# Performance work log

Measured on AMD Instinct MI355X. Metric: run time of the kernel, lower is better.

The kernel has to match this reference:

```python
import jax, jax.numpy as jnp
import numpy as np

N_NODES = 50000
N_EDGES = 800000
N_GRAPHS = 256
F_IN = 32
HEADS = 8
NEG_SLOPE = 0.2


def gat_conv(x, W, a_src, a_dst, bias, src, dst, n_nodes, heads, ch):
    # x: [N, Fin], W: [Fin, heads*ch], a_src/a_dst: [heads, ch], bias: [heads*ch]
    h = (x @ W).reshape(n_nodes, heads, ch)              # [N,H,C]
    alpha_src = jnp.sum(h * a_src, axis=-1)              # [N,H]
    alpha_dst = jnp.sum(h * a_dst, axis=-1)              # [N,H]
    logit = alpha_src[src] + alpha_dst[dst]              # [E,H]
    logit = jax.nn.leaky_relu(logit, NEG_SLOPE)
    # segment softmax over edges grouped by destination node
    m = jax.ops.segment_max(logit, dst, num_segments=n_nodes)   # [N,H]
    m = jnp.where(jnp.isfinite(m), m, 0.0)
    e = jnp.exp(logit - m[dst])                          # [E,H]
    denom = jax.ops.segment_sum(e, dst, num_segments=n_nodes)   # [N,H]
    alpha = e / (denom[dst] + 1e-16)                     # [E,H]
    msg = h[src] * alpha[:, :, None]                     # [E,H,C]
    out = jax.ops.segment_sum(msg, dst, num_segments=n_nodes)   # [N,H,C]
    return out.reshape(n_nodes, heads * ch) + bias


def setup_inputs() -> dict:
    key = jax.random.key(0)
    ks = jax.random.split(key, 20)
    H = HEADS
    glorot = lambda k, shape: jax.random.normal(k, shape, jnp.float32) * (2.0 / (shape[0] + shape[-1])) ** 0.5
    inp = {
        "x": jax.random.normal(ks[0], (N_NODES, F_IN), jnp.float32),
        "W1": glorot(ks[1], (F_IN, H * 8)),
        "a_src1": glorot(ks[2], (H, 8)),
        "a_dst1": glorot(ks[3], (H, 8)),
        "b1": jnp.zeros((H * 8,), jnp.float32),
        "W2": glorot(ks[4], (64, H * 16)),
        "a_src2": glorot(ks[5], (H, 16)),
        "a_dst2": glorot(ks[6], (H, 16)),
        "b2": jnp.zeros((H * 16,), jnp.float32),
        "W3": glorot(ks[7], (128, H * 16)),
        "a_src3": glorot(ks[8], (H, 16)),
        "a_dst3": glorot(ks[9], (H, 16)),
        "b3": jnp.zeros((H * 16,), jnp.float32),
        "fc1_w": glorot(ks[10], (128, 10)),
        "fc1_b": jnp.zeros((10,), jnp.float32),
        "fc2_w": glorot(ks[11], (10, 1)),
        "fc2_b": jnp.zeros((1,), jnp.float32),
        "edge_index": jax.random.randint(ks[12], (2, N_EDGES), 0, N_NODES, jnp.int64 if jax.config.jax_enable_x64 else jnp.int32),
        "batch_vec": jnp.sort(jax.random.randint(ks[13], (N_NODES,), 0, N_GRAPHS, jnp.int32)),
        "num_graphs": N_GRAPHS,
    }
    return inp


def reference(x, W1, a_src1, a_dst1, b1, W2, a_src2, a_dst2, b2,
              W3, a_src3, a_dst3, b3, fc1_w, fc1_b, fc2_w, fc2_b,
              edge_index, batch_vec, num_graphs):
    n = x.shape[0]
    loops = jnp.arange(n, dtype=edge_index.dtype)
    src = jnp.concatenate([edge_index[0], loops])  # PyG GATConv add_self_loops=True
    dst = jnp.concatenate([edge_index[1], loops])

    h = jax.nn.elu(gat_conv(x, W1, a_src1, a_dst1, b1, src, dst, n, HEADS, 8))
    h = jax.nn.elu(gat_conv(h, W2, a_src2, a_dst2, b2, src, dst, n, HEADS, 16))
    h = jax.nn.elu(gat_conv(h, W3, a_src3, a_dst3, b3, src, dst, n, HEADS, 16))

    # global mean pool over graphs
    sums = jax.ops.segment_sum(h, batch_vec, num_segments=num_graphs)
    counts = jax.ops.segment_sum(jnp.ones((n,), h.dtype), batch_vec, num_segments=num_graphs)
    pooled = sums / jnp.maximum(counts, 1.0)[:, None]   # [G,128]

    z = jax.nn.relu(pooled @ fc1_w + fc1_b)
    return z @ fc2_w + fc2_b                             # [G,1]
```

## Files before the change

kernel.cpp:

```cpp
#include <hip/hip_runtime.h>
#include <hip/hip_bf16.h>

#define N_NODES   50000
#define N_EDGES   800000
#define N_TOT     850000
#define N_GRAPHS  256
#define HEADS     8
#define NEG_SLOPE 0.2f

template<int FIN, int FOUT>
__global__ __launch_bounds__(256) void gemm_kernel(const float* __restrict__ X,
                                                   const float* __restrict__ W,
                                                   float* __restrict__ H) {
    constexpr int KC    = 32;
    constexpr int THR_F = FOUT / 4;
    constexpr int NPT   = 64 / (256 / THR_F);
    constexpr int XS_S  = 68;
    __shared__ float xs[KC * XS_S];
    __shared__ float ws[KC * FOUT];
    const int t = threadIdx.x;
    const int node0 = blockIdx.x * 64;
    const int fo  = (t % THR_F) * 4;
    const int ndb = (t / THR_F) * NPT;
    float4 acc[NPT];
#pragma unroll
    for (int i = 0; i < NPT; ++i) acc[i] = make_float4(0.f, 0.f, 0.f, 0.f);

    const int xn = t >> 2, ks = (t & 3) * 8;
    for (int kc = 0; kc < FIN; kc += KC) {
        __syncthreads();
        float4 a0 = make_float4(0.f,0.f,0.f,0.f), a1 = a0;
        if (node0 + xn < N_NODES) {
            const float* xp = X + (size_t)(node0 + xn) * FIN + kc + ks;
            a0 = *(const float4*)xp;
            a1 = *(const float4*)(xp + 4);
        }
        xs[(ks + 0) * XS_S + xn] = a0.x;
        xs[(ks + 1) * XS_S + xn] = a0.y;
        xs[(ks + 2) * XS_S + xn] = a0.z;
        xs[(ks + 3) * XS_S + xn] = a0.w;
        xs[(ks + 4) * XS_S + xn] = a1.x;
        xs[(ks + 5) * XS_S + xn] = a1.y;
        xs[(ks + 6) * XS_S + xn] = a1.z;
        xs[(ks + 7) * XS_S + xn] = a1.w;
        constexpr int WF4 = KC * FOUT / 4 / 256;
        const float4* wsrc = (const float4*)(W + (size_t)kc * FOUT);
        float4* wdst = (float4*)ws;
#pragma unroll
        for (int i = 0; i < WF4; ++i) wdst[t * WF4 + i] = wsrc[t * WF4 + i];
        __syncthreads();
#pragma unroll 4
        for (int k = 0; k < KC; ++k) {
            float4 wv = *(const float4*)(ws + k * FOUT + fo);
#pragma unroll
            for (int q = 0; q < NPT / 4; ++q) {
                float4 xv = *(const float4*)(xs + k * XS_S + ndb + q * 4);
                acc[q*4+0].x += xv.x * wv.x; acc[q*4+0].y += xv.x * wv.y;
                acc[q*4+0].z += xv.x * wv.z; acc[q*4+0].w += xv.x * wv.w;
                acc[q*4+1].x += xv.y * wv.x; acc[q*4+1].y += xv.y * wv.y;
                acc[q*4+1].z += xv.y * wv.z; acc[q*4+1].w += xv.y * wv.w;
                acc[q*4+2].x += xv.z * wv.x; acc[q*4+2].y += xv.z * wv.y;
                acc[q*4+2].z += xv.z * wv.z; acc[q*4+2].w += xv.z * wv.w;
                acc[q*4+3].x += xv.w * wv.x; acc[q*4+3].y += xv.w * wv.y;
                acc[q*4+3].z += xv.w * wv.z; acc[q*4+3].w += xv.w * wv.w;
            }
        }
    }
#pragma unroll
    for (int i = 0; i < NPT; ++i) {
        int row = node0 + ndb + i;
        if (row < N_NODES) *(float4*)(H + (size_t)row * FOUT + fo) = acc[i];
    }
}

template<int CH>
__global__ void alpha_kernel(const float* __restrict__ H,
                             const float* __restrict__ a_src,
                             const float* __restrict__ a_dst,
                             float* __restrict__ asrc, float* __restrict__ adst) {
    int tid = blockIdx.x * blockDim.x + threadIdx.x;
    if (tid >= N_NODES * HEADS) return;
    int n = tid / HEADS, h = tid % HEADS;
    const float4* hp = (const float4*)(H + (size_t)n * (HEADS * CH) + h * CH);
    const float4* as = (const float4*)(a_src + h * CH);
    const float4* ad = (const float4*)(a_dst + h * CH);
    float s = 0.f, d = 0.f;
#pragma unroll
    for (int c = 0; c < CH / 4; ++c) {
        float4 v = hp[c], a = as[c], b = ad[c];
        s += v.x * a.x + v.y * a.y + v.z * a.z + v.w * a.w;
        d += v.x * b.x + v.y * b.y + v.z * b.z + v.w * b.w;
    }
    asrc[tid] = s;
    adst[tid] = d;
}

__global__ void hist_kernel(const int* __restrict__ edst, int* __restrict__ cnt) {
    int e = blockIdx.x * blockDim.x + threadIdx.x;
    if (e >= N_TOT) return;
    int d = (e < N_EDGES) ? edst[e] : e - N_EDGES;
    atomicAdd(&cnt[d], 1);
}

__global__ void scan1_kernel(const int* __restrict__ cnt, int* __restrict__ excl,
                             int* __restrict__ bsum) {
    __shared__ int sm[256];
    int t = threadIdx.x;
    int i = blockIdx.x * 256 + t;
    int v = (i < N_NODES) ? cnt[i] : 0;
    sm[t] = v;
    __syncthreads();
    for (int off = 1; off < 256; off <<= 1) {
        int x = (t >= off) ? sm[t - off] : 0;
        __syncthreads();
        sm[t] += x;
        __syncthreads();
    }
    if (i < N_NODES) excl[i] = sm[t] - v;
    if (t == 255) bsum[blockIdx.x] = sm[255];
}

__global__ void scan2_kernel(int* __restrict__ bsum, int nblk) {
    __shared__ int sm[256];
    int t = threadIdx.x;
    int v = (t < nblk) ? bsum[t] : 0;
    sm[t] = v;
    __syncthreads();
    for (int off = 1; off < 256; off <<= 1) {
        int x = (t >= off) ? sm[t - off] : 0;
        __syncthreads();
        sm[t] += x;
        __syncthreads();
    }
    if (t < nblk) bsum[t] = sm[t] - v;
}

__global__ void scan3_kernel(const int* __restrict__ excl, const int* __restrict__ bsum,
                             int* __restrict__ row_ptr) {
    int i = blockIdx.x * blockDim.x + threadIdx.x;
    if (i < N_NODES) row_ptr[i] = excl[i] + bsum[i >> 8];
    if (i == N_NODES) row_ptr[N_NODES] = N_TOT;
}

__global__ void scatter_kernel(const int* __restrict__ esrc, const int* __restrict__ edst,
                               const int* __restrict__ row_ptr, int* __restrict__ cursor,
                               int* __restrict__ edge_src) {
    int e = blockIdx.x * blockDim.x + threadIdx.x;
    if (e >= N_TOT) return;
    int s, d;
    if (e < N_EDGES) { s = esrc[e]; d = edst[e]; } else { s = d = e - N_EDGES; }
    int pos = row_ptr[d] + atomicAdd(&cursor[d], 1);
    edge_src[pos] = s;
}

template<int CH>
__global__ __launch_bounds__(256) void gat_gather_kernel(
        const int* __restrict__ row_ptr, const int* __restrict__ edge_src,
        const float* __restrict__ asrc, const float* __restrict__ adst,
        const float* __restrict__ H, const float* __restrict__ bias,
        float* __restrict__ out) {
    constexpr int LPE   = 2 * CH;
    constexpr int SPLIT = 64 / LPE;
    constexpr int LPH   = CH / 4;
    constexpr int HS    = 8 * CH;
    const int n = (blockIdx.x * blockDim.x + threadIdx.x) >> 6;
    if (n >= N_NODES) return;
    const int lane = threadIdx.x & 63;
    const int sub = lane / LPE;
    const int li  = lane & (LPE - 1);
    const int h   = li / LPH;
    const int off = h * CH + (li & (LPH - 1)) * 4;
    const float adst_h = adst[n * 8 + h];
    const int e0 = row_ptr[n], e1 = row_ptr[n + 1];
    float sum = 0.f;
    float4 acc = make_float4(0.f, 0.f, 0.f, 0.f);
    int e = e0 + sub;
    for (; e + SPLIT < e1; e += 2 * SPLIT) {
        int s0 = edge_src[e];
        int s1 = edge_src[e + SPLIT];
        float l0 = asrc[s0 * 8 + h] + adst_h;
        float l1 = asrc[s1 * 8 + h] + adst_h;
        float4 h0 = *(const float4*)(H + (size_t)s0 * HS + off);
        float4 h1 = *(const float4*)(H + (size_t)s1 * HS + off);
        l0 = l0 > 0.f ? l0 : NEG_SLOPE * l0;
        l1 = l1 > 0.f ? l1 : NEG_SLOPE * l1;
        float w0 = __expf(l0), w1 = __expf(l1);
        sum += w0 + w1;
        acc.x += w0 * h0.x + w1 * h1.x;
        acc.y += w0 * h0.y + w1 * h1.y;
        acc.z += w0 * h0.z + w1 * h1.z;
        acc.w += w0 * h0.w + w1 * h1.w;
    }
    if (e < e1) {
        int s = edge_src[e];
        float l = asrc[s * 8 + h] + adst_h;
        float4 hv = *(const float4*)(H + (size_t)s * HS + off);
        l = l > 0.f ? l : NEG_SLOPE * l;
        float w = __expf(l);
        sum += w;
        acc.x += w * hv.x;
        acc.y += w * hv.y;
        acc.z += w * hv.z;
        acc.w += w * hv.w;
    }
#pragma unroll
    for (int mask = LPE; mask < 64; mask <<= 1) {
        sum   += __shfl_xor(sum, mask, 64);
        acc.x += __shfl_xor(acc.x, mask, 64);
        acc.y += __shfl_xor(acc.y, mask, 64);
        acc.z += __shfl_xor(acc.z, mask, 64);
        acc.w += __shfl_xor(acc.w, mask, 64);
    }
    float inv = 1.0f / (sum + 1e-16f);
    float4 bv = *(const float4*)(bias + off);
    float4 v;
    v.x = acc.x * inv + bv.x;  v.x = v.x > 0.f ? v.x : expm1f(v.x);
    v.y = acc.y * inv + bv.y;  v.y = v.y > 0.f ? v.y : expm1f(v.y);
    v.z = acc.z * inv + bv.z;  v.z = v.z > 0.f ? v.z : expm1f(v.z);
    v.w = acc.w * inv + bv.w;  v.w = v.w > 0.f ? v.w : expm1f(v.w);
    *(float4*)(out + (size_t)n * HS + off) = v;
}

__global__ void gstart_kernel(const int* __restrict__ batch, int* __restrict__ gstart) {
    int g = threadIdx.x;
    int lo = 0, hi = N_NODES;
    while (lo < hi) {
        int mid = (lo + hi) >> 1;
        if (batch[mid] < g) lo = mid + 1; else hi = mid;
    }
    gstart[g] = lo;
    if (g == 0) gstart[N_GRAPHS] = N_NODES;
}

__global__ __launch_bounds__(512) void pool_head_kernel(
        const float* __restrict__ act, const int* __restrict__ gstart,
        const float* __restrict__ fc1_w, const float* __restrict__ fc1_b,
        const float* __restrict__ fc2_w, const float* __restrict__ fc2_b,
        float* __restrict__ out) {
    int g = blockIdx.x;
    int t = threadIdx.x;
    int f = t & 127, strip = t >> 7;
    int n0 = gstart[g], n1 = gstart[g + 1];
    float s = 0.f;
    for (int n = n0 + strip; n < n1; n += 4) s += act[(size_t)n * 128 + f];
    __shared__ float sm[4][128];
    __shared__ float zz[10];
    sm[strip][f] = s;
    __syncthreads();
    if (strip == 0) {
        float cnt = (float)(n1 - n0);
        cnt = cnt > 1.f ? cnt : 1.f;
        sm[0][f] = (sm[0][f] + sm[1][f] + sm[2][f] + sm[3][f]) / cnt;
    }
    __syncthreads();
    if (t < 10) {
        float z = fc1_b[t];
        for (int q = 0; q < 128; ++q) z += sm[0][q] * fc1_w[q * 10 + t];
        zz[t] = z > 0.f ? z : 0.f;
    }
    __syncthreads();
    if (t == 0) {
        float o = fc2_b[0];
#pragma unroll
        for (int j = 0; j < 10; ++j) o += zz[j] * fc2_w[j];
        out[g] = o;
    }
}

extern "C" void kernel_launch(void* const* d_in, const int* in_sizes, int n_in,
                              void* d_out, int out_size, void* d_ws, size_t ws_size,
                              hipStream_t stream) {
    const float* x      = (const float*)d_in[0];
    const float* W1     = (const float*)d_in[1];
    const float* a_src1 = (const float*)d_in[2];
    const float* a_dst1 = (const float*)d_in[3];
    const float* b1     = (const float*)d_in[4];
    const float* W2     = (const float*)d_in[5];
    const float* a_src2 = (const float*)d_in[6];
    const float* a_dst2 = (const float*)d_in[7];
    const float* b2     = (const float*)d_in[8];
    const float* W3     = (const float*)d_in[9];
    const float* a_src3 = (const float*)d_in[10];
    const float* a_dst3 = (const float*)d_in[11];
    const float* b3     = (const float*)d_in[12];
    const float* fc1_w  = (const float*)d_in[13];
    const float* fc1_b  = (const float*)d_in[14];
    const float* fc2_w  = (const float*)d_in[15];
    const float* fc2_b  = (const float*)d_in[16];
    const int*   eidx   = (const int*)d_in[17];
    const int*   batch  = (const int*)d_in[18];
    const int* esrc = eidx;
    const int* edst = eidx + N_EDGES;
    float* out = (float*)d_out;

    float* ws      = (float*)d_ws;
    float* h_buf   = ws;
    float* act0    = h_buf + 6400000;
    float* act1    = act0 + 6400000;
    float* asrcb   = act1 + 6400000;
    float* adstb   = asrcb + 400000;
    int*   cnt     = (int*)(adstb + 400000);
    int*   excl    = cnt + 50000;
    int*   bsum    = excl + 50000;
    int*   row_ptr = bsum + 256;
    int*   cursor  = row_ptr + 50001;
    int*   edge_src= cursor + 50000;
    int*   gstart  = edge_src + 850000;

    const int B = 256;
    dim3 blk(B);
    dim3 g_gemm((N_NODES + 63) / 64);
    dim3 g_alpha((N_NODES * HEADS + B - 1) / B);
    dim3 g_edge((N_TOT + B - 1) / B);
    dim3 g_gather((N_NODES * 64 + B - 1) / B);
    const int nblk_scan = (N_NODES + 255) / 256;

    hipMemsetAsync(cnt, 0, 50000 * 4, stream);
    hipMemsetAsync(cursor, 0, 50000 * 4, stream);
    hist_kernel<<<g_edge, blk, 0, stream>>>(edst, cnt);
    scan1_kernel<<<dim3(nblk_scan), blk, 0, stream>>>(cnt, excl, bsum);
    scan2_kernel<<<dim3(1), blk, 0, stream>>>(bsum, nblk_scan);
    scan3_kernel<<<dim3((N_NODES + B) / B), blk, 0, stream>>>(excl, bsum, row_ptr);
    scatter_kernel<<<g_edge, blk, 0, stream>>>(esrc, edst, row_ptr, cursor, edge_src);
    gstart_kernel<<<dim3(1), blk, 0, stream>>>(batch, gstart);

    gemm_kernel<32, 64><<<g_gemm, blk, 0, stream>>>(x, W1, h_buf);
    alpha_kernel<8><<<g_alpha, blk, 0, stream>>>(h_buf, a_src1, a_dst1, asrcb, adstb);
    gat_gather_kernel<8><<<g_gather, blk, 0, stream>>>(row_ptr, edge_src, asrcb, adstb,
                                                       h_buf, b1, act0);

    gemm_kernel<64, 128><<<g_gemm, blk, 0, stream>>>(act0, W2, h_buf);
    alpha_kernel<16><<<g_alpha, blk, 0, stream>>>(h_buf, a_src2, a_dst2, asrcb, adstb);
    gat_gather_kernel<16><<<g_gather, blk, 0, stream>>>(row_ptr, edge_src, asrcb, adstb,
                                                        h_buf, b2, act1);

    gemm_kernel<128, 128><<<g_gemm, blk, 0, stream>>>(act1, W3, h_buf);
    alpha_kernel<16><<<g_alpha, blk, 0, stream>>>(h_buf, a_src3, a_dst3, asrcb, adstb);
    gat_gather_kernel<16><<<g_gather, blk, 0, stream>>>(row_ptr, edge_src, asrcb, adstb,
                                                        h_buf, b3, act0);

    pool_head_kernel<<<dim3(N_GRAPHS), dim3(512), 0, stream>>>(act0, gstart, fc1_w, fc1_b,
                                                               fc2_w, fc2_b, out);
}
```

Baseline: 372.0 us.

## Fuse attention-logit projection into GEMM epilogue and unroll gather by four

The per-layer alpha kernel is removed. The GEMM epilogue now computes the source and destination attention dot products from its accumulators, using lane shuffles to reduce across the threads that own one head. The edge gather loop is unrolled from two to four edges per iteration to keep more independent loads in flight, and the tail becomes a loop. The two workspace memsets are merged into one by placing the cursor buffer next to the count buffer. Together these save three kernel launches and a re-read of H, at the cost of more registers in the gather and GEMM kernels.

```diff
diff --git a/kernel.cpp b/kernel.cpp
--- a/kernel.cpp
+++ b/kernel.cpp
@@ -11,11 +11,16 @@
 template<int FIN, int FOUT>
 __global__ __launch_bounds__(256) void gemm_kernel(const float* __restrict__ X,
                                                    const float* __restrict__ W,
-                                                   float* __restrict__ H) {
+                                                   float* __restrict__ H,
+                                                   const float* __restrict__ a_src,
+                                                   const float* __restrict__ a_dst,
+                                                   float* __restrict__ asrc_o,
+                                                   float* __restrict__ adst_o) {
     constexpr int KC    = 32;
     constexpr int THR_F = FOUT / 4;
     constexpr int NPT   = 64 / (256 / THR_F);
     constexpr int XS_S  = 68;
+    constexpr int CH    = FOUT / 8;
     __shared__ float xs[KC * XS_S];
     __shared__ float ws[KC * FOUT];
     const int t = threadIdx.x;
@@ -66,33 +71,24 @@
             }
         }
     }
+    const int h   = fo / CH;
+    const float4 asv = *(const float4*)(a_src + h * CH + (fo % CH));
+    const float4 adv = *(const float4*)(a_dst + h * CH + (fo % CH));
+    constexpr int LPH = CH / 4;
 #pragma unroll
     for (int i = 0; i < NPT; ++i) {
         int row = node0 + ndb + i;
         if (row < N_NODES) *(float4*)(H + (size_t)row * FOUT + fo) = acc[i];
-    }
-}
-
-template<int CH>
-__global__ void alpha_kernel(const float* __restrict__ H,
-                             const float* __restrict__ a_src,
-                             const float* __restrict__ a_dst,
-                             float* __restrict__ asrc, float* __restrict__ adst) {
-    int tid = blockIdx.x * blockDim.x + threadIdx.x;
-    if (tid >= N_NODES * HEADS) return;
-    int n = tid / HEADS, h = tid % HEADS;
-    const float4* hp = (const float4*)(H + (size_t)n * (HEADS * CH) + h * CH);
-    const float4* as = (const float4*)(a_src + h * CH);
-    const float4* ad = (const float4*)(a_dst + h * CH);
-    float s = 0.f, d = 0.f;
-#pragma unroll
-    for (int c = 0; c < CH / 4; ++c) {
-        float4 v = hp[c], a = as[c], b = ad[c];
-        s += v.x * a.x + v.y * a.y + v.z * a.z + v.w * a.w;
-        d += v.x * b.x + v.y * b.y + v.z * b.z + v.w * b.w;
-    }
-    asrc[tid] = s;
-    adst[tid] = d;
+        float s = acc[i].x*asv.x + acc[i].y*asv.y + acc[i].z*asv.z + acc[i].w*asv.w;
+        float d = acc[i].x*adv.x + acc[i].y*adv.y + acc[i].z*adv.z + acc[i].w*adv.w;
+        s += __shfl_xor(s, 1, 64);
+        d += __shfl_xor(d, 1, 64);
+        if (LPH == 4) { s += __shfl_xor(s, 2, 64); d += __shfl_xor(d, 2, 64); }
+        if ((t & (LPH - 1)) == 0 && row < N_NODES) {
+            asrc_o[row * 8 + h] = s;
+            adst_o[row * 8 + h] = d;
+        }
+    }
 }
 
 __global__ void hist_kernel(const int* __restrict__ edst, int* __restrict__ cnt) {
@@ -175,23 +171,31 @@
     float sum = 0.f;
     float4 acc = make_float4(0.f, 0.f, 0.f, 0.f);
     int e = e0 + sub;
-    for (; e + SPLIT < e1; e += 2 * SPLIT) {
+    for (; e + 3 * SPLIT < e1; e += 4 * SPLIT) {
         int s0 = edge_src[e];
         int s1 = edge_src[e + SPLIT];
+        int s2 = edge_src[e + 2 * SPLIT];
+        int s3 = edge_src[e + 3 * SPLIT];
         float l0 = asrc[s0 * 8 + h] + adst_h;
         float l1 = asrc[s1 * 8 + h] + adst_h;
+        float l2 = asrc[s2 * 8 + h] + adst_h;
+        float l3 = asrc[s3 * 8 + h] + adst_h;
         float4 h0 = *(const float4*)(H + (size_t)s0 * HS + off);
         float4 h1 = *(const float4*)(H + (size_t)s1 * HS + off);
+        float4 h2 = *(const float4*)(H + (size_t)s2 * HS + off);
+        float4 h3 = *(const float4*)(H + (size_t)s3 * HS + off);
         l0 = l0 > 0.f ? l0 : NEG_SLOPE * l0;
         l1 = l1 > 0.f ? l1 : NEG_SLOPE * l1;
-        float w0 = __expf(l0), w1 = __expf(l1);
-        sum += w0 + w1;
-        acc.x += w0 * h0.x + w1 * h1.x;
-        acc.y += w0 * h0.y + w1 * h1.y;
-        acc.z += w0 * h0.z + w1 * h1.z;
-        acc.w += w0 * h0.w + w1 * h1.w;
-    }
-    if (e < e1) {
+        l2 = l2 > 0.f ? l2 : NEG_SLOPE * l2;
+        l3 = l3 > 0.f ? l3 : NEG_SLOPE * l3;
+        float w0 = __expf(l0), w1 = __expf(l1), w2 = __expf(l2), w3 = __expf(l3);
+        sum += (w0 + w1) + (w2 + w3);
+        acc.x += w0 * h0.x + w1 * h1.x + w2 * h2.x + w3 * h3.x;
+        acc.y += w0 * h0.y + w1 * h1.y + w2 * h2.y + w3 * h3.y;
+        acc.z += w0 * h0.z + w1 * h1.z + w2 * h2.z + w3 * h3.z;
+        acc.w += w0 * h0.w + w1 * h1.w + w2 * h2.w + w3 * h3.w;
+    }
+    for (; e < e1; e += SPLIT) {
         int s = edge_src[e];
         float l = asrc[s * 8 + h] + adst_h;
         float4 hv = *(const float4*)(H + (size_t)s * HS + off);
@@ -300,23 +304,21 @@
     float* asrcb   = act1 + 6400000;
     float* adstb   = asrcb + 400000;
     int*   cnt     = (int*)(adstb + 400000);
-    int*   excl    = cnt + 50000;
+    int*   cursor  = cnt + 50000;
+    int*   excl    = cursor + 50000;
     int*   bsum    = excl + 50000;
     int*   row_ptr = bsum + 256;
-    int*   cursor  = row_ptr + 50001;
-    int*   edge_src= cursor + 50000;
+    int*   edge_src= row_ptr + 50001;
     int*   gstart  = edge_src + 850000;
 
     const int B = 256;
     dim3 blk(B);
     dim3 g_gemm((N_NODES + 63) / 64);
-    dim3 g_alpha((N_NODES * HEADS + B - 1) / B);
     dim3 g_edge((N_TOT + B - 1) / B);
     dim3 g_gather((N_NODES * 64 + B - 1) / B);
     const int nblk_scan = (N_NODES + 255) / 256;
 
-    hipMemsetAsync(cnt, 0, 50000 * 4, stream);
-    hipMemsetAsync(cursor, 0, 50000 * 4, stream);
+    hipMemsetAsync(cnt, 0, 100000 * 4, stream);
     hist_kernel<<<g_edge, blk, 0, stream>>>(edst, cnt);
     scan1_kernel<<<dim3(nblk_scan), blk, 0, stream>>>(cnt, excl, bsum);
     scan2_kernel<<<dim3(1), blk, 0, stream>>>(bsum, nblk_scan);
@@ -324,18 +326,18 @@
     scatter_kernel<<<g_edge, blk, 0, stream>>>(esrc, edst, row_ptr, cursor, edge_src);
     gstart_kernel<<<dim3(1), blk, 0, stream>>>(batch, gstart);
 
-    gemm_kernel<32, 64><<<g_gemm, blk, 0, stream>>>(x, W1, h_buf);
-    alpha_kernel<8><<<g_alpha, blk, 0, stream>>>(h_buf, a_src1, a_dst1, asrcb, adstb);
+    gemm_kernel<32, 64><<<g_gemm, blk, 0, stream>>>(x, W1, h_buf, a_src1, a_dst1,
+                                                    asrcb, adstb);
     gat_gather_kernel<8><<<g_gather, blk, 0, stream>>>(row_ptr, edge_src, asrcb, adstb,
                                                        h_buf, b1, act0);
 
-    gemm_kernel<64, 128><<<g_gemm, blk, 0, stream>>>(act0, W2, h_buf);
-    alpha_kernel<16><<<g_alpha, blk, 0, stream>>>(h_buf, a_src2, a_dst2, asrcb, adstb);
+    gemm_kernel<64, 128><<<g_gemm, blk, 0, stream>>>(act0, W2, h_buf, a_src2, a_dst2,
+                                                     asrcb, adstb);
     gat_gather_kernel<16><<<g_gather, blk, 0, stream>>>(row_ptr, edge_src, asrcb, adstb,
                                                         h_buf, b2, act1);
 
-    gemm_kernel<128, 128><<<g_gemm, blk, 0, stream>>>(act1, W3, h_buf);
-    alpha_kernel<16><<<g_alpha, blk, 0, stream>>>(h_buf, a_src3, a_dst3, asrcb, adstb);
+    gemm_kernel<128, 128><<<g_gemm, blk, 0, stream>>>(act1, W3, h_buf, a_src3, a_dst3,
+                                                      asrcb, adstb);
     gat_gather_kernel<16><<<g_gather, blk, 0, stream>>>(row_ptr, edge_src, asrcb, adstb,
                                                         h_buf, b3, act0);
 
```

Result: faster. 349.1 us (-6.1%).
